# Performance work log

Measured on AMD Instinct MI355X. Metric: run time of the kernel, lower is better.

The kernel has to match this reference:

```python
import jax, jax.numpy as jnp
import numpy as np

B, D, ND, N2, H = 16384, 512, 4, 32, 4
C = D  # attention channels (per-detector feature dim)
EPS = 1e-5


def setup_inputs() -> dict:
    key = jax.random.key(0)
    ks = jax.random.split(key, 8)
    rn = lambda k, s, sc: jax.random.normal(k, s, jnp.float32) * sc
    return {
        'x': jax.random.normal(ks[0], (B, D), jnp.float32),
        'bn1_g': jnp.ones(D * ND, jnp.float32), 'bn1_b': jnp.zeros(D * ND, jnp.float32),
        'w1': rn(ks[1], (ND, D, D), 1e-4),  # diagonal blocks of the masked EnsembleLinear weight
        'bn2_g': jnp.ones(D * ND, jnp.float32), 'bn2_b': jnp.zeros(D * ND, jnp.float32),
        'wq': rn(ks[2], (C, D), 0.02), 'bq': jnp.zeros(C, jnp.float32),
        'wk': rn(ks[3], (C, D), 0.02), 'bk': jnp.zeros(C, jnp.float32),
        'wv': rn(ks[4], (C, D), 0.02), 'bv': jnp.zeros(C, jnp.float32),
        'wo': rn(ks[5], (C, C), 0.02), 'bo': jnp.zeros(C, jnp.float32),
        'ln1_g': jnp.ones(C, jnp.float32), 'ln1_b': jnp.zeros(C, jnp.float32),
        'wff': rn(ks[6], (C, C), 0.02), 'bff': jnp.zeros(C, jnp.float32),
        'ln2_g': jnp.ones(C, jnp.float32), 'ln2_b': jnp.zeros(C, jnp.float32),
        'w2': rn(ks[7], (ND, N2, D), 1e-4),
        'bn3_g': jnp.ones(N2 * ND, jnp.float32), 'bn3_b': jnp.zeros(N2 * ND, jnp.float32),
    }


def _batchnorm(x, g, b):
    # training-mode BatchNorm1d: biased batch stats over the batch axis
    m = x.mean(0)
    v = ((x - m) ** 2).mean(0)
    return (x - m) * jax.lax.rsqrt(v + EPS) * g + b


def _layernorm(x, g, b):
    m = x.mean(-1, keepdims=True)
    v = ((x - m) ** 2).mean(-1, keepdims=True)
    return (x - m) * jax.lax.rsqrt(v + EPS) * g + b


def reference(x, bn1_g, bn1_b, w1, bn2_g, bn2_b, wq, bq, wk, bk, wv, bv, wo, bo,
              ln1_g, ln1_b, wff, bff, ln2_g, ln2_b, w2, bn3_g, bn3_b):
    n = x.shape[0]
    # concat x num_detectors times along features: [n, ND*D]
    xc = jnp.tile(x, (1, ND))
    h = _batchnorm(xc, bn1_g, bn1_b)
    # EnsembleLinear 1: block-diagonal masked matmul == one small GEMM per detector
    h = jnp.einsum('ndi,doi->ndo', h.reshape(n, ND, D), w1).reshape(n, ND * D)
    h = jax.nn.sigmoid(_batchnorm(h, bn2_g, bn2_b))
    # 4-token self-attention over detectors: t is [n, ND, D]
    t = h.reshape(n, ND, D)
    hd = C // H
    q = (t @ wq.T + bq).reshape(n, ND, H, hd).transpose(0, 2, 1, 3)  # [n,H,S,hd]
    k = (t @ wk.T + bk).reshape(n, ND, H, hd).transpose(0, 2, 1, 3)
    v = (t @ wv.T + bv).reshape(n, ND, H, hd).transpose(0, 2, 1, 3)
    scale = jnp.sqrt(jnp.float32(C / H))
    scores = jnp.einsum('nhqd,nhkd->nhqk', q, k) / scale
    attn = jax.nn.softmax(scores, axis=-1)
    o = jnp.einsum('nhqk,nhkd->nhqd', attn, v).transpose(0, 2, 1, 3).reshape(n, ND, C)
    o = o @ wo.T + bo
    a1 = _layernorm(o + t, ln1_g, ln1_b)
    a2 = _layernorm(a1 @ wff.T + bff + a1, ln2_g, ln2_b)
    # EnsembleLinear 2: per-detector D -> N2
    h2 = jnp.einsum('ndi,doi->ndo', a2, w2).reshape(n, ND * N2)
    out = jax.nn.sigmoid(_batchnorm(h2, bn3_g, bn3_b))
    return out
```

## Files before the change

### kernel.cpp

```cpp
#include <hip/hip_runtime.h>
#include <hip/hip_bf16.h>

#define EPS 1e-5f

typedef __attribute__((ext_vector_type(8))) short bf16x8;
typedef __attribute__((ext_vector_type(4))) float f32x4;
typedef __attribute__((ext_vector_type(4))) float float4v;

__device__ __forceinline__ float b2f(short u) {
    union { unsigned int i; float f; } x;
    x.i = ((unsigned int)(unsigned short)u) << 16;
    return x.f;
}
__device__ __forceinline__ short f2b(float f) {
    unsigned int x = __builtin_bit_cast(unsigned int, f);
    unsigned int r = (x + 0x7FFFu + ((x >> 16) & 1u)) >> 16;
    return (short)r;
}

__device__ __forceinline__ void load_lds16(const void* g, void* l) {
    __builtin_amdgcn_global_load_lds(
        (const __attribute__((address_space(1))) unsigned int*)g,
        (__attribute__((address_space(3))) unsigned int*)l, 16, 0, 0);
}


__device__ __forceinline__ void cast8(const float* __restrict__ src, short* __restrict__ dst, long idx) {
    const float4v* s = (const float4v*)src;
    float4v a = s[idx * 2], b = s[idx * 2 + 1];
    bf16x8 o;
    o[0] = f2b(a[0]); o[1] = f2b(a[1]); o[2] = f2b(a[2]); o[3] = f2b(a[3]);
    o[4] = f2b(b[0]); o[5] = f2b(b[1]); o[6] = f2b(b[2]); o[7] = f2b(b[3]);
    *(bf16x8*)(dst + idx * 8) = o;
}

__global__ __launch_bounds__(256) void k_prep(
    const float* __restrict__ wq, const float* __restrict__ wk, const float* __restrict__ wv,
    const float* __restrict__ wo, const float* __restrict__ wff, const float* __restrict__ w2,
    const float* __restrict__ bq, const float* __restrict__ bk, const float* __restrict__ bv,
    short* __restrict__ Wqkvb, short* __restrict__ wo_b, short* __restrict__ wff_b,
    short* __restrict__ w2_b, float* __restrict__ bqkv) {
    int bid = blockIdx.x, tid = threadIdx.x;
    if (bid < 640) {
        int seg = bid >> 7;
        long idx = (long)(bid & 127) * 256 + tid;
        const float* src;
        short* dst;
        if (seg == 0) { src = wq; dst = Wqkvb; }
        else if (seg == 1) { src = wk; dst = Wqkvb + 262144; }
        else if (seg == 2) { src = wv; dst = Wqkvb + 524288; }
        else if (seg == 3) { src = wo; dst = wo_b; }
        else { src = wff; dst = wff_b; }
        cast8(src, dst, idx);
    } else if (bid < 672) {
        long idx = (long)(bid - 640) * 256 + tid;
        cast8(w2, w2_b, idx);
    } else {
        int i = (bid - 672) * 256 + tid;
        if (i < 512) bqkv[i] = bq[i];
        else if (i < 1024) bqkv[i] = bk[i - 512];
        else if (i < 1536) bqkv[i] = bv[i - 1024];
    }
}

__global__ __launch_bounds__(256) void k_statcast_x(const float* __restrict__ x,
                                                    short* __restrict__ xb,
                                                    float* __restrict__ psum, float* __restrict__ psq) {
    int b = blockIdx.x, tid = threadIdx.x;
    const float* xp = x + (long)b * 64 * 512;
    short* xo = xb + (long)b * 64 * 512;
    float s0 = 0, q0 = 0, s1 = 0, q1 = 0;
    for (int r = 0; r < 64; ++r) {
        float v0 = xp[r * 512 + tid];
        float v1 = xp[r * 512 + tid + 256];
        xo[r * 512 + tid] = f2b(v0);
        xo[r * 512 + tid + 256] = f2b(v1);
        s0 += v0; q0 += v0 * v0; s1 += v1; q1 += v1 * v1;
    }
    psum[b * 512 + tid] = s0; psum[b * 512 + tid + 256] = s1;
    psq[b * 512 + tid] = q0;  psq[b * 512 + tid + 256] = q1;
}


__global__ __launch_bounds__(256) void k_finalize_meanrs(const float* __restrict__ psum,
                                                         const float* __restrict__ psq,
                                                         int nparts, int ncols, float invB,
                                                         float* __restrict__ mean, float* __restrict__ rs) {
    int l = threadIdx.x & 63, grp = threadIdx.x >> 6;
    int c = blockIdx.x * 64 + l;
    float s = 0, q = 0;
    for (int p = grp; p < nparts; p += 4) {
        s += psum[(long)p * ncols + c];
        q += psq[(long)p * ncols + c];
    }
    __shared__ float rs_[4][64], rq_[4][64];
    rs_[grp][l] = s; rq_[grp][l] = q;
    __syncthreads();
    if (grp == 0) {
        s = rs_[0][l] + rs_[1][l] + rs_[2][l] + rs_[3][l];
        q = rq_[0][l] + rq_[1][l] + rq_[2][l] + rq_[3][l];
        float m = s * invB;
        float v = q * invB - m * m;
        mean[c] = m;
        rs[c] = rsqrtf(v + EPS);
    }
}

__global__ __launch_bounds__(256) void k_finalize_ss(const float* __restrict__ psum,
                                                     const float* __restrict__ psq,
                                                     int nparts, int ncols, float invB,
                                                     const float* __restrict__ g, const float* __restrict__ bb,
                                                     float* __restrict__ scale, float* __restrict__ shift) {
    int l = threadIdx.x & 63, grp = threadIdx.x >> 6;
    int c = blockIdx.x * 64 + l;
    float s = 0, q = 0;
    for (int p = grp; p < nparts; p += 4) {
        s += psum[(long)p * ncols + c];
        q += psq[(long)p * ncols + c];
    }
    __shared__ float rs_[4][64], rq_[4][64];
    rs_[grp][l] = s; rq_[grp][l] = q;
    __syncthreads();
    if (grp == 0) {
        s = rs_[0][l] + rs_[1][l] + rs_[2][l] + rs_[3][l];
        q = rq_[0][l] + rq_[1][l] + rq_[2][l] + rq_[3][l];
        float m = s * invB, v = q * invB - m * m;
        float sc = g[c] * rsqrtf(v + EPS);
        scale[c] = sc;
        shift[c] = bb[c] - m * sc;
    }
}

__global__ __launch_bounds__(256) void k_fold_w1(const float* __restrict__ w1, const float* __restrict__ g1,
                                                 const float* __restrict__ b1, const float* __restrict__ mean,
                                                 const float* __restrict__ rs,
                                                 short* __restrict__ W1b, float* __restrict__ beff) {
    int bx = blockIdx.x;
    int d = bx >> 9, tid = threadIdx.x;
    const float* wrow = w1 + (long)bx * 512;
    float part = 0.f;
    for (int i = tid; i < 512; i += 256) {
        float wv = wrow[i];
        float sc = rs[i] * g1[d * 512 + i];
        W1b[(long)bx * 512 + i] = f2b(wv * sc);
        part += (b1[d * 512 + i] - mean[i] * sc) * wv;
    }
    __shared__ float red[256];
    red[tid] = part;
    __syncthreads();
    for (int st = 128; st > 0; st >>= 1) {
        if (tid < st) red[tid] += red[tid + st];
        __syncthreads();
    }
    if (tid == 0) beff[bx] = red[0];
}

__global__ __launch_bounds__(256) void k_bnsig(const short* h, short* t,
                                               const float* __restrict__ scale,
                                               const float* __restrict__ shift) {
    long i8 = ((long)blockIdx.x * 256 + threadIdx.x) * 8;
    int c0 = (int)(i8 & 2047);
    bf16x8 v = *(const bf16x8*)(h + i8);
    bf16x8 o;
#pragma unroll
    for (int j = 0; j < 8; ++j) {
        float x = b2f(v[j]) * scale[c0 + j] + shift[c0 + j];
        o[j] = f2b(1.f / (1.f + __expf(-x)));
    }
    *(bf16x8*)(t + i8) = o;
}

__global__ __launch_bounds__(256) void k_ln(const short* in, short* out,
                                            const float* __restrict__ g, const float* __restrict__ bb) {
    int w = threadIdx.x >> 6, lane = threadIdx.x & 63;
    long row = (long)blockIdx.x * 4 + w;
    const short* rp = in + row * 512;
    bf16x8 v = *(const bf16x8*)(rp + lane * 8);
    float f[8];
    float s = 0.f;
#pragma unroll
    for (int j = 0; j < 8; ++j) { f[j] = b2f(v[j]); s += f[j]; }
#pragma unroll
    for (int m = 1; m < 64; m <<= 1) s += __shfl_xor(s, m, 64);
    float mean = s * (1.f / 512.f);
    float q = 0.f;
#pragma unroll
    for (int j = 0; j < 8; ++j) { float d = f[j] - mean; q += d * d; }
#pragma unroll
    for (int m = 1; m < 64; m <<= 1) q += __shfl_xor(q, m, 64);
    float rs = rsqrtf(q * (1.f / 512.f) + EPS);
    bf16x8 o;
#pragma unroll
    for (int j = 0; j < 8; ++j) {
        int c = lane * 8 + j;
        o[j] = f2b((f[j] - mean) * rs * g[c] + bb[c]);
    }
    *(bf16x8*)(out + row * 512 + lane * 8) = o;
}

__global__ __launch_bounds__(256) void k_stats_o(const float* __restrict__ pre,
                                                 float* __restrict__ psum, float* __restrict__ psq) {
    int b = blockIdx.x, tid = threadIdx.x;
    int c = tid & 127, rh = tid >> 7;
    const float* pp = pre + (long)b * 128 * 128;
    float s = 0, q = 0;
    for (int r = rh; r < 128; r += 2) {
        float v = pp[r * 128 + c];
        s += v; q += v * v;
    }
    psum[(b * 2 + rh) * 128 + c] = s;
    psq[(b * 2 + rh) * 128 + c] = q;
}

__global__ __launch_bounds__(256) void k_bn3sig(const float* __restrict__ pre, float* __restrict__ out,
                                                const float* __restrict__ scale, const float* __restrict__ shift) {
    long i4 = ((long)blockIdx.x * 256 + threadIdx.x) * 4;
    float4v v = *(const float4v*)(pre + i4);
    int c0 = (int)(i4 & 127);
    float4v o;
#pragma unroll
    for (int j = 0; j < 4; ++j) {
        float x = v[j] * scale[c0 + j] + shift[c0 + j];
        o[j] = 1.f / (1.f + __expf(-x));
    }
    *(float4v*)(out + i4) = o;
}


template <int BM, int BN, int WGM, int WGN, bool ADD_RES, bool OUT_BF16>
__global__ __launch_bounds__(WGM* WGN * 64) void k_gemm_bt(
    const short* __restrict__ A, int a_zoff, int lda,
    const short* __restrict__ W, int w_zoff,
    const float* __restrict__ bias, int bias_zoff,
    short* Cb, float* Cf, int c_zoff, int ldc,
    const short* R, int ldr, int K) {
    constexpr int BK = 32;
    constexpr int WM = BM / WGM, WN = BN / WGN;
    constexpr int AM = WM / 16, AN = WN / 16;
    constexpr int NT = WGM * WGN * 64;
    constexpr int CH = (BM + BN) * (BK / 8);

    __shared__ alignas(16) short Smem[(BM + BN) * BK];

    int tid = threadIdx.x;
    int wave = tid >> 6, lane = tid & 63;
    int wm = (wave % WGM) * WM, wn = (wave / WGM) * WN;
    long m0 = (long)blockIdx.x * BM;
    int n0 = blockIdx.y * BN;
    int z = blockIdx.z;
    const short* Az = A + (long)z * a_zoff;
    const short* Wz = W + (long)z * w_zoff;

    f32x4 acc[AM][AN];
#pragma unroll
    for (int i = 0; i < AM; ++i)
#pragma unroll
        for (int j = 0; j < AN; ++j)
#pragma unroll
            for (int q = 0; q < 4; ++q) acc[i][j][q] = 0.f;

    int fr = lane & 15, ko = (lane >> 4) * 8;

    for (int k0 = 0; k0 < K; k0 += BK) {
#pragma unroll
        for (int c = tid; c < CH; c += NT) {
            int row = c >> 2, koff = (c & 3) * 8;
            const short* g = (row < BM) ? (Az + (m0 + row) * lda + k0 + koff)
                                        : (Wz + (long)(n0 + row - BM) * K + k0 + koff);
            load_lds16(g, (char*)Smem + (size_t)c * 16);
        }
        __syncthreads();
        bf16x8 af[AM], bfr[AN];
#pragma unroll
        for (int i = 0; i < AM; ++i) af[i] = *(const bf16x8*)(&Smem[(wm + i * 16 + fr) * BK + ko]);
#pragma unroll
        for (int j = 0; j < AN; ++j) bfr[j] = *(const bf16x8*)(&Smem[(BM + wn + j * 16 + fr) * BK + ko]);
#pragma unroll
        for (int i = 0; i < AM; ++i)
#pragma unroll
            for (int j = 0; j < AN; ++j)
                acc[i][j] = __builtin_amdgcn_mfma_f32_16x16x32_bf16(af[i], bfr[j], acc[i][j], 0, 0, 0);
        __syncthreads();
    }

    int cr = (lane >> 4) * 4, cc = lane & 15;
#pragma unroll
    for (int i = 0; i < AM; ++i) {
#pragma unroll
        for (int j = 0; j < AN; ++j) {
            int col = n0 + wn + j * 16 + cc;
            float bv = bias ? bias[(long)z * bias_zoff + col] : 0.f;
#pragma unroll
            for (int q = 0; q < 4; ++q) {
                long row = m0 + wm + i * 16 + cr + q;
                float v = acc[i][j][q] + bv;
                if constexpr (ADD_RES) v += b2f(R[row * (long)ldr + col]);
                long idx = row * (long)ldc + (long)z * c_zoff + col;
                if constexpr (OUT_BF16) Cb[idx] = f2b(v);
                else Cf[idx] = v;
            }
        }
    }
}


__global__ __launch_bounds__(256) void k_gemm_e1(
    const short* __restrict__ A, const short* __restrict__ W1, const float* __restrict__ beff,
    short* __restrict__ h, float* __restrict__ psum, float* __restrict__ psq) {
    constexpr int BK = 32;
    __shared__ alignas(16) short Smem[256 * BK];
    __shared__ float cS[2][128], cQ[2][128];

    int tid = threadIdx.x;
    int wave = tid >> 6, lane = tid & 63;
    int wm = (wave & 1) * 64, wn = (wave >> 1) * 64;
    long m0 = (long)blockIdx.x * 128;
    int n0 = blockIdx.y * 128;
    int z = blockIdx.z;
    const short* Wz = W1 + (long)z * 512 * 512;

    f32x4 acc[4][4];
#pragma unroll
    for (int i = 0; i < 4; ++i)
#pragma unroll
        for (int j = 0; j < 4; ++j)
#pragma unroll
            for (int q = 0; q < 4; ++q) acc[i][j][q] = 0.f;

    int fr = lane & 15, ko = (lane >> 4) * 8;

    for (int k0 = 0; k0 < 512; k0 += BK) {
#pragma unroll
        for (int c = tid; c < 1024; c += 256) {
            int row = c >> 2, koff = (c & 3) * 8;
            const short* g = (row < 128) ? (A + (m0 + row) * 512 + k0 + koff)
                                         : (Wz + (long)(n0 + row - 128) * 512 + k0 + koff);
            load_lds16(g, (char*)Smem + (size_t)c * 16);
        }
        __syncthreads();
        bf16x8 af[4], bfr[4];
#pragma unroll
        for (int i = 0; i < 4; ++i) af[i] = *(const bf16x8*)(&Smem[(wm + i * 16 + fr) * BK + ko]);
#pragma unroll
        for (int j = 0; j < 4; ++j) bfr[j] = *(const bf16x8*)(&Smem[(128 + wn + j * 16 + fr) * BK + ko]);
#pragma unroll
        for (int i = 0; i < 4; ++i)
#pragma unroll
            for (int j = 0; j < 4; ++j)
                acc[i][j] = __builtin_amdgcn_mfma_f32_16x16x32_bf16(af[i], bfr[j], acc[i][j], 0, 0, 0);
        __syncthreads();
    }

    int cr = (lane >> 4) * 4, cc = lane & 15;
    float bv[4], colS[4], colQ[4];
#pragma unroll
    for (int j = 0; j < 4; ++j) {
        bv[j] = beff[z * 512 + n0 + wn + j * 16 + cc];
        colS[j] = 0.f; colQ[j] = 0.f;
    }
#pragma unroll
    for (int i = 0; i < 4; ++i)
#pragma unroll
        for (int j = 0; j < 4; ++j)
#pragma unroll
            for (int q = 0; q < 4; ++q) {
                float v = acc[i][j][q] + bv[j];
                acc[i][j][q] = v;
                colS[j] += v; colQ[j] += v * v;
            }
#pragma unroll
    for (int i = 0; i < 4; ++i)
#pragma unroll
        for (int q = 0; q < 4; ++q) {
            long row = m0 + wm + i * 16 + cr + q;
            short* hp = h + row * 2048 + z * 512 + n0 + wn + cc;
#pragma unroll
            for (int j = 0; j < 4; ++j) hp[j * 16] = f2b(acc[i][j][q]);
        }
#pragma unroll
    for (int j = 0; j < 4; ++j) {
        float s = colS[j], qq = colQ[j];
        s += __shfl_xor(s, 16, 64); s += __shfl_xor(s, 32, 64);
        qq += __shfl_xor(qq, 16, 64); qq += __shfl_xor(qq, 32, 64);
        if (lane < 16) { cS[wave & 1][wn + j * 16 + cc] = s; cQ[wave & 1][wn + j * 16 + cc] = qq; }
    }
    __syncthreads();
    if (tid < 128) {
        float S = cS[0][tid] + cS[1][tid];
        float Q = cQ[0][tid] + cQ[1][tid];
        psum[(long)blockIdx.x * 2048 + z * 512 + n0 + tid] = S;
        psq[(long)blockIdx.x * 2048 + z * 512 + n0 + tid] = Q;
    }
}

__global__ __launch_bounds__(256) void k_attn(const short* __restrict__ qkv, short* __restrict__ ao) {
    __shared__ alignas(16) short lds[4][4][1544];
    __shared__ float attn_s[4][4][4][4];
    int w = threadIdx.x >> 6, lane = threadIdx.x & 63;
    long n = (long)blockIdx.x * 4 + w;
    const short* src = qkv + n * 4 * 1536;
#pragma unroll
    for (int c = 0; c < 12; ++c) {
        int e = c * 512 + lane * 8;
        *(bf16x8*)(&lds[w][e / 1536][e % 1536]) = *(const bf16x8*)(src + e);
    }
    __syncthreads();
    int h = lane >> 4, a = (lane >> 2) & 3, b = lane & 3;
    const short* qp = &lds[w][a][h * 128];
    const short* kp = &lds[w][b][512 + h * 128];
    float s = 0.f;
#pragma unroll
    for (int j = 0; j < 128; j += 8) {
        bf16x8 qv = *(const bf16x8*)(qp + j);
        bf16x8 kv = *(const bf16x8*)(kp + j);
#pragma unroll
        for (int x = 0; x < 8; ++x) s += b2f(qv[x]) * b2f(kv[x]);
    }
    s *= 0.08838834764831845f;
    float mx = fmaxf(s, __shfl_xor(s, 1, 64));
    mx = fmaxf(mx, __shfl_xor(mx, 2, 64));
    float e = __expf(s - mx);
    float den = e + __shfl_xor(e, 1, 64);
    den += __shfl_xor(den, 2, 64);
    attn_s[w][h][a][b] = e / den;
    __syncthreads();
    int ta = lane >> 4, cg = lane & 15;
#pragma unroll
    for (int hh = 0; hh < 4; ++hh) {
        int c0 = hh * 128 + cg * 8;
        float at0 = attn_s[w][hh][ta][0], at1 = attn_s[w][hh][ta][1];
        float at2 = attn_s[w][hh][ta][2], at3 = attn_s[w][hh][ta][3];
        bf16x8 v0 = *(const bf16x8*)(&lds[w][0][1024 + c0]);
        bf16x8 v1 = *(const bf16x8*)(&lds[w][1][1024 + c0]);
        bf16x8 v2 = *(const bf16x8*)(&lds[w][2][1024 + c0]);
        bf16x8 v3 = *(const bf16x8*)(&lds[w][3][1024 + c0]);
        bf16x8 ov;
#pragma unroll
        for (int j = 0; j < 8; ++j) {
            float val = at0 * b2f(v0[j]) + at1 * b2f(v1[j]) + at2 * b2f(v2[j]) + at3 * b2f(v3[j]);
            ov[j] = f2b(val);
        }
        *(bf16x8*)(ao + (n * 4 + ta) * 512 + c0) = ov;
    }
}


extern "C" void kernel_launch(void* const* d_in, const int* in_sizes, int n_in,
                              void* d_out, int out_size, void* d_ws, size_t ws_size,
                              hipStream_t stream) {
    const float* x = (const float*)d_in[0];
    const float* bn1_g = (const float*)d_in[1];
    const float* bn1_b = (const float*)d_in[2];
    const float* w1 = (const float*)d_in[3];
    const float* bn2_g = (const float*)d_in[4];
    const float* bn2_b = (const float*)d_in[5];
    const float* wq = (const float*)d_in[6];
    const float* bq = (const float*)d_in[7];
    const float* wk = (const float*)d_in[8];
    const float* bk = (const float*)d_in[9];
    const float* wv = (const float*)d_in[10];
    const float* bv = (const float*)d_in[11];
    const float* wo = (const float*)d_in[12];
    const float* bo = (const float*)d_in[13];
    const float* ln1_g = (const float*)d_in[14];
    const float* ln1_b = (const float*)d_in[15];
    const float* wff = (const float*)d_in[16];
    const float* bff = (const float*)d_in[17];
    const float* ln2_g = (const float*)d_in[18];
    const float* ln2_b = (const float*)d_in[19];
    const float* w2 = (const float*)d_in[20];
    const float* bn3_g = (const float*)d_in[21];
    const float* bn3_b = (const float*)d_in[22];
    float* out = (float*)d_out;

    char* ws = (char*)d_ws;
    size_t off = 0;
    auto alloc = [&](size_t bytes) {
        void* p = ws + off;
        off = (off + bytes + 255) & ~(size_t)255;
        return p;
    };

    short* W1b = (short*)alloc(4l * 512 * 512 * 2);
    float* beff = (float*)alloc(4l * 512 * 4);
    short* Wqkvb = (short*)alloc(1536l * 512 * 2);
    float* bqkv = (float*)alloc(1536l * 4);
    short* wo_b = (short*)alloc(512l * 512 * 2);
    short* wff_b = (short*)alloc(512l * 512 * 2);
    short* w2_b = (short*)alloc(4l * 32 * 512 * 2);
    float* mean1 = (float*)alloc(512 * 4);
    float* rs1 = (float*)alloc(512 * 4);
    float* scale2 = (float*)alloc(2048 * 4);
    float* shift2 = (float*)alloc(2048 * 4);
    float* scale3 = (float*)alloc(128 * 4);
    float* shift3 = (float*)alloc(128 * 4);
    float* psum1 = (float*)alloc(256l * 512 * 4);
    float* psq1 = (float*)alloc(256l * 512 * 4);
    float* psum2 = (float*)alloc(128l * 2048 * 4);
    float* psq2 = (float*)alloc(128l * 2048 * 4);
    float* psum3 = (float*)alloc(256l * 128 * 4);
    float* psq3 = (float*)alloc(256l * 128 * 4);
    short* slotA = (short*)alloc(16384l * 2048 * 2);
    float* out_pre = (float*)alloc(16384l * 128 * 4);
    short* bufB = (short*)alloc(16384l * 2048 * 2);

    long NCq = 1024;
    for (long cand = 4096; cand >= 1024; cand >>= 1) {
        if (off + (size_t)cand * 12288 + (1u << 20) <= ws_size) { NCq = cand; break; }
    }
    char* arena = (char*)alloc((size_t)NCq * 12288);
    short* xb = (short*)arena;
    short* qkv_c = (short*)arena;
    xb = bufB;

    dim3 B256(256);

    hipLaunchKernelGGL(k_prep, dim3(678), B256, 0, stream,
                       wq, wk, wv, wo, wff, w2, bq, bk, bv,
                       Wqkvb, wo_b, wff_b, w2_b, bqkv);
    hipLaunchKernelGGL(k_statcast_x, dim3(256), B256, 0, stream, x, xb, psum1, psq1);

    hipLaunchKernelGGL(k_finalize_meanrs, dim3(8), B256, 0, stream, psum1, psq1, 256, 512,
                       1.f / 16384.f, mean1, rs1);
    hipLaunchKernelGGL(k_fold_w1, dim3(2048), B256, 0, stream, w1, bn1_g, bn1_b, mean1, rs1, W1b, beff);

    hipLaunchKernelGGL(k_gemm_e1, dim3(128, 4, 4), B256, 0, stream,
                       xb, W1b, beff, slotA, psum2, psq2);

    hipLaunchKernelGGL(k_finalize_ss, dim3(32), B256, 0, stream, psum2, psq2, 128, 2048,
                       1.f / 16384.f, bn2_g, bn2_b, scale2, shift2);
    hipLaunchKernelGGL(k_bnsig, dim3(16384), B256, 0, stream, slotA, slotA, scale2, shift2);

    long nch = 16384 / NCq;
    for (long c = 0; c < nch; ++c) {
        long r0 = c * NCq;
        const short* t_c = slotA + r0 * 2048;
        int gx = (int)(NCq * 4 / 128);

        hipLaunchKernelGGL((k_gemm_bt<128, 128, 2, 2, false, true>), dim3(gx, 12, 1), B256, 0, stream,
                           t_c, 0, 512, Wqkvb, 0, bqkv, 0,
                           qkv_c, (float*)nullptr, 0, 1536, (const short*)nullptr, 0, 512);

        hipLaunchKernelGGL(k_attn, dim3((int)(NCq / 4)), B256, 0, stream,
                           qkv_c, bufB + r0 * 2048);
    }

    hipLaunchKernelGGL((k_gemm_bt<128, 128, 2, 2, true, true>), dim3(512, 4, 1), B256, 0, stream,
                       bufB, 0, 512, wo_b, 0, bo, 0,
                       slotA, (float*)nullptr, 0, 512, slotA, 512, 512);

    hipLaunchKernelGGL(k_ln, dim3(16384), B256, 0, stream, slotA, slotA, ln1_g, ln1_b);

    hipLaunchKernelGGL((k_gemm_bt<128, 128, 2, 2, true, true>), dim3(512, 4, 1), B256, 0, stream,
                       slotA, 0, 512, wff_b, 0, bff, 0,
                       bufB, (float*)nullptr, 0, 512, slotA, 512, 512);

    hipLaunchKernelGGL(k_ln, dim3(16384), B256, 0, stream, bufB, bufB, ln2_g, ln2_b);

    hipLaunchKernelGGL((k_gemm_bt<128, 32, 4, 1, false, false>), dim3(128, 1, 4), B256, 0, stream,
                       bufB, 512, 2048, w2_b, 32 * 512, (const float*)nullptr, 0,
                       (short*)nullptr, out_pre, 32, 128, (const short*)nullptr, 0, 512);

    hipLaunchKernelGGL(k_stats_o, dim3(128), B256, 0, stream, out_pre, psum3, psq3);
    hipLaunchKernelGGL(k_finalize_ss, dim3(2), B256, 0, stream, psum3, psq3, 256, 128,
                       1.f / 16384.f, bn3_g, bn3_b, scale3, shift3);
    hipLaunchKernelGGL(k_bn3sig, dim3(2048), B256, 0, stream, out_pre, out, scale3, shift3);
}
```

Baseline: 618.1 us.

## Run BN-sigmoid, attention, FFN and output GEMM per chunk in a cache-resident arena

Moves the BN2-sigmoid, output projection, both layernorms, FFN GEMM and final ensemble GEMM into the per-chunk loop, so intermediates live in a small reusable arena instead of full-size buffers. The full-batch bufB buffer is removed. The goal is to keep chunk working sets in the last-level cache and cut HBM traffic between stages. In exchange there are more kernel launches and smaller grids per launch.

```diff
diff --git a/kernel.cpp b/kernel.cpp
--- a/kernel.cpp
+++ b/kernel.cpp
@@ -502,16 +502,16 @@
     float* psq3 = (float*)alloc(256l * 128 * 4);
     short* slotA = (short*)alloc(16384l * 2048 * 2);
     float* out_pre = (float*)alloc(16384l * 128 * 4);
-    short* bufB = (short*)alloc(16384l * 2048 * 2);
 
     long NCq = 1024;
     for (long cand = 4096; cand >= 1024; cand >>= 1) {
-        if (off + (size_t)cand * 12288 + (1u << 20) <= ws_size) { NCq = cand; break; }
-    }
-    char* arena = (char*)alloc((size_t)NCq * 12288);
+        if (off + (size_t)cand * 20480 + (1u << 20) <= ws_size) { NCq = cand; break; }
+    }
+    char* arena = (char*)alloc((size_t)NCq * 20480);
+    short* qkv_c = (short*)arena;
+    short* attn_c = (short*)(arena + (size_t)NCq * 12288);
+    short* a2_c = (short*)(arena + (size_t)NCq * 16384);
     short* xb = (short*)arena;
-    short* qkv_c = (short*)arena;
-    xb = bufB;
 
     dim3 B256(256);
 
@@ -529,37 +529,37 @@
 
     hipLaunchKernelGGL(k_finalize_ss, dim3(32), B256, 0, stream, psum2, psq2, 128, 2048,
                        1.f / 16384.f, bn2_g, bn2_b, scale2, shift2);
-    hipLaunchKernelGGL(k_bnsig, dim3(16384), B256, 0, stream, slotA, slotA, scale2, shift2);
 
     long nch = 16384 / NCq;
     for (long c = 0; c < nch; ++c) {
         long r0 = c * NCq;
-        const short* t_c = slotA + r0 * 2048;
+        short* t_c = slotA + r0 * 2048;
         int gx = (int)(NCq * 4 / 128);
+
+        hipLaunchKernelGGL(k_bnsig, dim3((int)NCq), B256, 0, stream, t_c, t_c, scale2, shift2);
 
         hipLaunchKernelGGL((k_gemm_bt<128, 128, 2, 2, false, true>), dim3(gx, 12, 1), B256, 0, stream,
                            t_c, 0, 512, Wqkvb, 0, bqkv, 0,
                            qkv_c, (float*)nullptr, 0, 1536, (const short*)nullptr, 0, 512);
 
-        hipLaunchKernelGGL(k_attn, dim3((int)(NCq / 4)), B256, 0, stream,
-                           qkv_c, bufB + r0 * 2048);
-    }
-
-    hipLaunchKernelGGL((k_gemm_bt<128, 128, 2, 2, true, true>), dim3(512, 4, 1), B256, 0, stream,
-                       bufB, 0, 512, wo_b, 0, bo, 0,
-                       slotA, (float*)nullptr, 0, 512, slotA, 512, 512);
-
-    hipLaunchKernelGGL(k_ln, dim3(16384), B256, 0, stream, slotA, slotA, ln1_g, ln1_b);
-
-    hipLaunchKernelGGL((k_gemm_bt<128, 128, 2, 2, true, true>), dim3(512, 4, 1), B256, 0, stream,
-                       slotA, 0, 512, wff_b, 0, bff, 0,
-                       bufB, (float*)nullptr, 0, 512, slotA, 512, 512);
-
-    hipLaunchKernelGGL(k_ln, dim3(16384), B256, 0, stream, bufB, bufB, ln2_g, ln2_b);
-
-    hipLaunchKernelGGL((k_gemm_bt<128, 32, 4, 1, false, false>), dim3(128, 1, 4), B256, 0, stream,
-                       bufB, 512, 2048, w2_b, 32 * 512, (const float*)nullptr, 0,
-                       (short*)nullptr, out_pre, 32, 128, (const short*)nullptr, 0, 512);
+        hipLaunchKernelGGL(k_attn, dim3((int)(NCq / 4)), B256, 0, stream, qkv_c, attn_c);
+
+        hipLaunchKernelGGL((k_gemm_bt<128, 128, 2, 2, true, true>), dim3(gx, 4, 1), B256, 0, stream,
+                           attn_c, 0, 512, wo_b, 0, bo, 0,
+                           t_c, (float*)nullptr, 0, 512, t_c, 512, 512);
+
+        hipLaunchKernelGGL(k_ln, dim3((int)NCq), B256, 0, stream, t_c, t_c, ln1_g, ln1_b);
+
+        hipLaunchKernelGGL((k_gemm_bt<128, 128, 2, 2, true, true>), dim3(gx, 4, 1), B256, 0, stream,
+                           t_c, 0, 512, wff_b, 0, bff, 0,
+                           a2_c, (float*)nullptr, 0, 512, t_c, 512, 512);
+
+        hipLaunchKernelGGL(k_ln, dim3((int)NCq), B256, 0, stream, a2_c, a2_c, ln2_g, ln2_b);
+
+        hipLaunchKernelGGL((k_gemm_bt<128, 32, 4, 1, false, false>), dim3((int)(NCq / 128), 1, 4), B256, 0, stream,
+                           a2_c, 512, 2048, w2_b, 32 * 512, (const float*)nullptr, 0,
+                           (short*)nullptr, out_pre + r0 * 128, 32, 128, (const short*)nullptr, 0, 512);
+    }
 
     hipLaunchKernelGGL(k_stats_o, dim3(128), B256, 0, stream, out_pre, psum3, psq3);
     hipLaunchKernelGGL(k_finalize_ss, dim3(2), B256, 0, stream, psum3, psq3, 256, 128,
```

New measurement: 703.1 us. 13.8% more time.
